# Optimization experiments

Measured on AMD Instinct MI355X. Metric: run time of the kernel, lower is better.

## Reference

```python
import jax, jax.numpy as jnp
import numpy as np


def setup_inputs() -> dict:
    key = jax.random.key(0)
    k0, k1, k2, k3, k4 = jax.random.split(key, 5)
    T, B, S, H = 32, 8192, 256, 128
    return {
        "states_batch": jax.random.normal(k0, (T, B, S), dtype=jnp.float32),
        "W1": jax.random.normal(k1, (T, S, H), dtype=jnp.float32) * (S ** -0.5),
        "b1": jax.random.normal(k2, (T, H), dtype=jnp.float32) * 0.01,
        "W2": jax.random.normal(k3, (T, H, 1), dtype=jnp.float32) * 0.01,
        "b2": jax.random.normal(k4, (T, 1), dtype=jnp.float32) * 0.01,
    }


def reference(states_batch, W1, b1, W2, b2):
    # [T,B,S] @ [T,S,H] -> [T,B,H], bias, SiLU
    h = jnp.einsum('tbs,tsh->tbh', states_batch, W1) + b1[:, None, :]
    h = jax.nn.silu(h)
    # [T,B,H] @ [T,H,1] -> [T,B,1], bias, squeeze -> [T,B]
    out = jnp.einsum('tbh,tho->tbo', h, W2) + b2[:, None, :]
    return out.squeeze(-1)
```

## Files before the change

### kernel.cpp

```cpp
#include <hip/hip_runtime.h>
#include <hip/hip_bf16.h>

typedef __attribute__((ext_vector_type(8))) short bf16x8;
typedef __attribute__((ext_vector_type(4))) float f32x4;

#define T_DIM 32
#define B_DIM 8192
#define S_DIM 256
#define H_DIM 128
#define BM    64
#define NCH   8
#define BLOCKS_PER_T 16

__device__ __forceinline__ uint32_t cvt_pk_bf16(float lo, float hi) {
  uint32_t r;
  asm("v_cvt_pk_bf16_f32 %0, %1, %2" : "=v"(r) : "v"(lo), "v"(hi));
  return r;
}

__global__ __launch_bounds__(256, 2) void cvar_mlp_kernel(
    const float* __restrict__ states, const float* __restrict__ W1,
    const float* __restrict__ b1, const float* __restrict__ W2,
    const float* __restrict__ b2, float* __restrict__ out)
{
  __shared__ __align__(16) char lds[2][BM * 512];
  __shared__ float red[2][4][BM];

  const int tid  = threadIdx.x;
  const int wid  = tid >> 6;
  const int lane = tid & 63;
  const int l15  = lane & 15;
  const int lg   = lane >> 4;

  const int bidx = blockIdx.x;
  const int xcd  = bidx & 7;
  const int slot = bidx >> 3;
  const int t    = xcd * 4 + (slot >> 4);
  const int cg   = slot & 15;
  const int b0   = cg * (BM * NCH);

  const float*  Ag  = states + ((size_t)t * B_DIM + b0) * S_DIM;
  const float4* A4  = reinterpret_cast<const float4*>(Ag);
  const float*  W1g = W1 + (size_t)t * (S_DIM * H_DIM);

  float4 av[16];
#pragma unroll
  for (int i = 0; i < 16; ++i)
    av[i] = A4[i * 256 + tid];

  bf16x8 bfr[2][8];
#pragma unroll
  for (int nloc = 0; nloc < 2; ++nloc) {
    const int ncol = (wid * 2 + nloc) * 16 + l15;
#pragma unroll
    for (int ks = 0; ks < 8; ++ks) {
      const int kbase = ks * 32 + lg * 8;
      float e[8];
#pragma unroll
      for (int j = 0; j < 8; ++j)
        e[j] = W1g[(size_t)(kbase + j) * H_DIM + ncol];
      union { uint32_t u[4]; bf16x8 v; } uu;
      uu.u[0] = cvt_pk_bf16(e[0], e[1]);
      uu.u[1] = cvt_pk_bf16(e[2], e[3]);
      uu.u[2] = cvt_pk_bf16(e[4], e[5]);
      uu.u[3] = cvt_pk_bf16(e[6], e[7]);
      bfr[nloc][ks] = uu.v;
    }
  }

  float b1c[2], w2c[2];
#pragma unroll
  for (int nloc = 0; nloc < 2; ++nloc) {
    const int col = (wid * 2 + nloc) * 16 + l15;
    b1c[nloc] = b1[(size_t)t * H_DIM + col];
    w2c[nloc] = W2[(size_t)t * H_DIM + col];
  }
  const float b2t = b2[t];
  float* outt = out + (size_t)t * B_DIM + b0;

#pragma unroll
  for (int i = 0; i < 16; ++i) {
    const int f   = i * 256 + tid;
    const int row = f >> 6;
    const int kq  = f & 63;
    const uint32_t lo = cvt_pk_bf16(av[i].x, av[i].y);
    const uint32_t hi = cvt_pk_bf16(av[i].z, av[i].w);
    int byteoff = row * 512 + kq * 8;
    byteoff ^= (row & 7) << 4;
    *reinterpret_cast<uint2*>(&lds[0][byteoff]) = make_uint2(lo, hi);
  }
  __syncthreads();

  for (int c = 0; c < NCH; ++c) {
    const int cur = c & 1;

    if (c + 1 < NCH) {
#pragma unroll
      for (int i = 0; i < 16; ++i)
        av[i] = A4[(c + 1) * (BM * S_DIM / 4) + i * 256 + tid];
    }

    f32x4 acc[4][2];
#pragma unroll
    for (int mt = 0; mt < 4; ++mt)
#pragma unroll
      for (int nloc = 0; nloc < 2; ++nloc)
        acc[mt][nloc] = (f32x4){0.f, 0.f, 0.f, 0.f};

#pragma unroll
    for (int mt = 0; mt < 4; ++mt) {
      const int row = mt * 16 + l15;
      bf16x8 afr[8];
#pragma unroll
      for (int ks = 0; ks < 8; ++ks) {
        int byteoff = row * 512 + ks * 64 + lg * 16;
        byteoff ^= (row & 7) << 4;
        afr[ks] = *reinterpret_cast<const bf16x8*>(&lds[cur][byteoff]);
      }
#pragma unroll
      for (int ks = 0; ks < 8; ++ks) {
        acc[mt][0] = __builtin_amdgcn_mfma_f32_16x16x32_bf16(afr[ks], bfr[0][ks], acc[mt][0], 0, 0, 0);
        acc[mt][1] = __builtin_amdgcn_mfma_f32_16x16x32_bf16(afr[ks], bfr[1][ks], acc[mt][1], 0, 0, 0);
      }
    }

#pragma unroll
    for (int mt = 0; mt < 4; ++mt) {
      float part[4];
#pragma unroll
      for (int r = 0; r < 4; ++r) {
        float s = 0.f;
#pragma unroll
        for (int nloc = 0; nloc < 2; ++nloc) {
          const float h   = acc[mt][nloc][r] + b1c[nloc];
          const float sig = 1.f / (1.f + __expf(-h));
          s += h * sig * w2c[nloc];
        }
        s += __shfl_xor(s, 1);
        s += __shfl_xor(s, 2);
        s += __shfl_xor(s, 4);
        s += __shfl_xor(s, 8);
        part[r] = s;
      }
      if (l15 == 0) {
#pragma unroll
        for (int r = 0; r < 4; ++r)
          red[cur][wid][mt * 16 + lg * 4 + r] = part[r];
      }
    }

    if (c + 1 < NCH) {
#pragma unroll
      for (int i = 0; i < 16; ++i) {
        const int f   = i * 256 + tid;
        const int row = f >> 6;
        const int kq  = f & 63;
        const uint32_t lo = cvt_pk_bf16(av[i].x, av[i].y);
        const uint32_t hi = cvt_pk_bf16(av[i].z, av[i].w);
        int byteoff = row * 512 + kq * 8;
        byteoff ^= (row & 7) << 4;
        *reinterpret_cast<uint2*>(&lds[cur ^ 1][byteoff]) = make_uint2(lo, hi);
      }
    }
    __syncthreads();

    if (tid < BM) {
      const float o = red[cur][0][tid] + red[cur][1][tid] +
                      red[cur][2][tid] + red[cur][3][tid] + b2t;
      outt[c * BM + tid] = o;
    }
  }
}

extern "C" void kernel_launch(void* const* d_in, const int* in_sizes, int n_in,
                              void* d_out, int out_size, void* d_ws, size_t ws_size,
                              hipStream_t stream) {
  const float* states = (const float*)d_in[0];
  const float* W1     = (const float*)d_in[1];
  const float* b1     = (const float*)d_in[2];
  const float* W2     = (const float*)d_in[3];
  const float* b2     = (const float*)d_in[4];
  float* out          = (float*)d_out;

  const int grid = T_DIM * BLOCKS_PER_T;
  cvar_mlp_kernel<<<grid, 256, 0, stream>>>(states, W1, b1, W2, b2, out);
}
```

Measured before the change: 55.45 us.

## Stream states directly to LDS via global_load_lds and convert to bf16 at read

Replaces the register-staged global load plus bf16 convert and LDS store with direct global-to-LDS DMA loads (global_load_lds, 16 bytes per lane) that keep fp32 in a swizzled LDS layout. The bf16 conversion moves to the LDS read side, before the MFMAs. The row tile is halved to 32 with twice as many chunks so the fp32 double buffer still fits in LDS. This frees the VGPRs that held the staged tile and removes the explicit store phase, at the cost of twice the LDS bytes read per chunk and extra per-chunk barriers.

```diff
diff --git a/kernel.cpp b/kernel.cpp
--- a/kernel.cpp
+++ b/kernel.cpp
@@ -8,9 +8,14 @@
 #define B_DIM 8192
 #define S_DIM 256
 #define H_DIM 128
-#define BM    64
-#define NCH   8
+#define BM    32
+#define NCH   16
 #define BLOCKS_PER_T 16
+
+#define GLD_LDS16(gsrc, ldst)                                                  \
+  __builtin_amdgcn_global_load_lds(                                            \
+      (const __attribute__((address_space(1))) void*)(gsrc),                   \
+      (__attribute__((address_space(3))) void*)(ldst), 16, 0, 0)
 
 __device__ __forceinline__ uint32_t cvt_pk_bf16(float lo, float hi) {
   uint32_t r;
@@ -23,7 +28,7 @@
     const float* __restrict__ b1, const float* __restrict__ W2,
     const float* __restrict__ b2, float* __restrict__ out)
 {
-  __shared__ __align__(16) char lds[2][BM * 512];
+  __shared__ __align__(16) float ldsA[2][BM * S_DIM];
   __shared__ float red[2][4][BM];
 
   const int tid  = threadIdx.x;
@@ -43,10 +48,13 @@
   const float4* A4  = reinterpret_cast<const float4*>(Ag);
   const float*  W1g = W1 + (size_t)t * (S_DIM * H_DIM);
 
-  float4 av[16];
 #pragma unroll
-  for (int i = 0; i < 16; ++i)
-    av[i] = A4[i * 256 + tid];
+  for (int i = 0; i < 8; ++i) {
+    const int rowt = i * 4 + wid;
+    const int sg   = lane ^ (rowt & 7);
+    GLD_LDS16(A4 + (size_t)0 * 2048 + rowt * 64 + sg,
+              &ldsA[0][(i * 256 + wid * 64) * 4]);
+  }
 
   bf16x8 bfr[2][8];
 #pragma unroll
@@ -78,17 +86,6 @@
   const float b2t = b2[t];
   float* outt = out + (size_t)t * B_DIM + b0;
 
-#pragma unroll
-  for (int i = 0; i < 16; ++i) {
-    const int f   = i * 256 + tid;
-    const int row = f >> 6;
-    const int kq  = f & 63;
-    const uint32_t lo = cvt_pk_bf16(av[i].x, av[i].y);
-    const uint32_t hi = cvt_pk_bf16(av[i].z, av[i].w);
-    int byteoff = row * 512 + kq * 8;
-    byteoff ^= (row & 7) << 4;
-    *reinterpret_cast<uint2*>(&lds[0][byteoff]) = make_uint2(lo, hi);
-  }
   __syncthreads();
 
   for (int c = 0; c < NCH; ++c) {
@@ -96,26 +93,39 @@
 
     if (c + 1 < NCH) {
 #pragma unroll
-      for (int i = 0; i < 16; ++i)
-        av[i] = A4[(c + 1) * (BM * S_DIM / 4) + i * 256 + tid];
+      for (int i = 0; i < 8; ++i) {
+        const int rowt = i * 4 + wid;
+        const int sg   = lane ^ (rowt & 7);
+        GLD_LDS16(A4 + (size_t)(c + 1) * 2048 + rowt * 64 + sg,
+                  &ldsA[cur ^ 1][(i * 256 + wid * 64) * 4]);
+      }
     }
 
-    f32x4 acc[4][2];
+    f32x4 acc[2][2];
 #pragma unroll
-    for (int mt = 0; mt < 4; ++mt)
+    for (int mt = 0; mt < 2; ++mt)
 #pragma unroll
       for (int nloc = 0; nloc < 2; ++nloc)
         acc[mt][nloc] = (f32x4){0.f, 0.f, 0.f, 0.f};
 
 #pragma unroll
-    for (int mt = 0; mt < 4; ++mt) {
-      const int row = mt * 16 + l15;
+    for (int mt = 0; mt < 2; ++mt) {
+      const int r = mt * 16 + l15;
+      const int m = r & 7;
       bf16x8 afr[8];
 #pragma unroll
       for (int ks = 0; ks < 8; ++ks) {
-        int byteoff = row * 512 + ks * 64 + lg * 16;
-        byteoff ^= (row & 7) << 4;
-        afr[ks] = *reinterpret_cast<const bf16x8*>(&lds[cur][byteoff]);
+        const int ga = ks * 8 + lg * 2;
+        const float4 f0 = *reinterpret_cast<const float4*>(
+            &ldsA[cur][r * S_DIM + ((ga    ) ^ m) * 4]);
+        const float4 f1 = *reinterpret_cast<const float4*>(
+            &ldsA[cur][r * S_DIM + ((ga + 1) ^ m) * 4]);
+        union { uint32_t u[4]; bf16x8 v; } uu;
+        uu.u[0] = cvt_pk_bf16(f0.x, f0.y);
+        uu.u[1] = cvt_pk_bf16(f0.z, f0.w);
+        uu.u[2] = cvt_pk_bf16(f1.x, f1.y);
+        uu.u[3] = cvt_pk_bf16(f1.z, f1.w);
+        afr[ks] = uu.v;
       }
 #pragma unroll
       for (int ks = 0; ks < 8; ++ks) {
@@ -125,7 +135,7 @@
     }
 
 #pragma unroll
-    for (int mt = 0; mt < 4; ++mt) {
+    for (int mt = 0; mt < 2; ++mt) {
       float part[4];
 #pragma unroll
       for (int r = 0; r < 4; ++r) {
@@ -149,19 +159,6 @@
       }
     }
 
-    if (c + 1 < NCH) {
-#pragma unroll
-      for (int i = 0; i < 16; ++i) {
-        const int f   = i * 256 + tid;
-        const int row = f >> 6;
-        const int kq  = f & 63;
-        const uint32_t lo = cvt_pk_bf16(av[i].x, av[i].y);
-        const uint32_t hi = cvt_pk_bf16(av[i].z, av[i].w);
-        int byteoff = row * 512 + kq * 8;
-        byteoff ^= (row & 7) << 4;
-        *reinterpret_cast<uint2*>(&lds[cur ^ 1][byteoff]) = make_uint2(lo, hi);
-      }
-    }
     __syncthreads();
 
     if (tid < BM) {
```

After: 65.49 us. 18.1% more time.
